# Kernel tuning notes

Hardware: AMD Instinct MI355X
Metric: run time of the kernel (lower is better)

Reference implementation:

```python
import jax, jax.numpy as jnp
import numpy as np

B, S, D, H = 4, 2048, 1024, 16
HD = D // H  # head_dim = 64
SCALE = HD ** -0.5


def setup_inputs() -> dict:
    key = jax.random.key(0)
    k1, k2, k3, k4, k5 = jax.random.split(key, 5)
    std = D ** -0.5
    return {
        "x": jax.random.normal(k1, (B, S, D), dtype=jnp.float32),
        "w_qkv": jax.random.normal(k2, (D, 3 * D), dtype=jnp.float32) * std,
        "b_qkv": jax.random.normal(k3, (3 * D,), dtype=jnp.float32) * 0.01,
        "w_out": jax.random.normal(k4, (D, D), dtype=jnp.float32) * std,
        "b_out": jax.random.normal(k5, (D,), dtype=jnp.float32) * 0.01,
    }


def reference(x, w_qkv, b_qkv, w_out, b_out):
    b, s, d = x.shape
    qkv = x @ w_qkv + b_qkv                                   # [B,S,3D]
    qkv = qkv.reshape(b, s, 3, H, HD).transpose(2, 0, 3, 1, 4)  # [3,B,H,S,HD]
    q, k, v = qkv[0], qkv[1], qkv[2]
    attn = jnp.einsum("bhqd,bhkd->bhqk", q, k) * SCALE        # [B,H,S,S]
    attn = jax.nn.softmax(attn, axis=-1)
    out = jnp.einsum("bhqk,bhkd->bhqd", attn, v)              # [B,H,S,HD]
    out = out.transpose(0, 2, 1, 3).reshape(b, s, d)          # [B,S,D]
    return out @ w_out + b_out
```

## Files before the change

### kernel.cpp

```cpp
#include <hip/hip_runtime.h>
#include <stdint.h>
#include <stddef.h>

#define NB 4
#define NS 2048
#define ND 1024
#define NH 16
#define HDIM 64
#define SCALE 0.125f

typedef __attribute__((ext_vector_type(4))) float f32x4;
typedef __attribute__((ext_vector_type(16))) float f32x16;
typedef __attribute__((ext_vector_type(8))) __bf16 bf16x8;
typedef __attribute__((ext_vector_type(4))) uint32_t u32x4;

__device__ __forceinline__ uint16_t f2bf(float f) {
  uint32_t u = __builtin_bit_cast(uint32_t, f);
  return (uint16_t)((u + 0x7fffu + ((u >> 16) & 1u)) >> 16);
}

__device__ __forceinline__ void gload_lds16(const void* g, void* l) {
  __builtin_amdgcn_global_load_lds((const __attribute__((address_space(1))) void*)g,
                                   (__attribute__((address_space(3))) void*)l, 16, 0, 0);
}

__device__ __forceinline__ uint32_t cvtpk(float lo, float hi) {
  uint32_t r;
  asm("v_cvt_pk_bf16_f32 %0, %1, %2" : "=v"(r) : "v"(lo), "v"(hi));
  return r;
}

__device__ __forceinline__ void permswap(uint32_t& a, uint32_t& b) {
  asm("v_permlane32_swap_b32 %0, %1" : "+v"(a), "+v"(b));
}

__device__ __forceinline__ float fexp2(float x) {
  float r;
  asm("v_exp_f32 %0, %1" : "=v"(r) : "v"(x));
  return r;
}

__global__ void k_cvt_bf16(const float* __restrict__ in, uint16_t* __restrict__ out, int n4) {
  int i = blockIdx.x * blockDim.x + threadIdx.x;
  if (i >= n4) return;
  float4 v = reinterpret_cast<const float4*>(in)[i];
  ushort4 o;
  o.x = f2bf(v.x); o.y = f2bf(v.y); o.z = f2bf(v.z); o.w = f2bf(v.w);
  reinterpret_cast<ushort4*>(out)[i] = o;
}

__global__ void k_transpose_cvt(const float* __restrict__ in, uint16_t* __restrict__ out,
                                int K, int N) {
  __shared__ float tile[64][65];
  const int nb = blockIdx.x * 64, kb = blockIdx.y * 64;
  const int c = threadIdx.x & 63, r0 = threadIdx.x >> 6;
#pragma unroll
  for (int i = 0; i < 16; ++i) {
    int r = r0 * 16 + i;
    tile[r][c] = in[(size_t)(kb + r) * N + nb + c];
  }
  __syncthreads();
#pragma unroll
  for (int i = 0; i < 16; ++i) {
    int rr = r0 * 16 + i;
    out[(size_t)(nb + rr) * K + kb + c] = f2bf(tile[c][rr]);
  }
}

__global__ void k_vt_repack(const uint16_t* __restrict__ qkv, uint16_t* __restrict__ vt) {
  __shared__ uint16_t tile[64][66];
  const int bh = blockIdx.y, sb = blockIdx.x * 64;
  const int b = bh >> 4, h = bh & 15;
  const int c = threadIdx.x & 63, r0 = threadIdx.x >> 6;
#pragma unroll
  for (int i = 0; i < 16; ++i) {
    int s = r0 * 16 + i;
    tile[s][c] = qkv[(size_t)(b * NS + sb + s) * 3072 + 2048 + h * 64 + c];
  }
  __syncthreads();
#pragma unroll
  for (int i = 0; i < 16; ++i) {
    int d = r0 * 16 + i;
    vt[(size_t)bh * 64 * NS + (size_t)d * NS + sb + c] = tile[c][d];
  }
}

template<int OUT_BF16>
__global__ __launch_bounds__(256)
void k_gemm(const uint16_t* __restrict__ A, const uint16_t* __restrict__ Bt,
            const float* __restrict__ bias, void* __restrict__ C,
            int M, int N, int K) {
  __shared__ __align__(16) char Al[8192];
  __shared__ __align__(16) char Bl[8192];
  const int tid = threadIdx.x;
  const int wave = tid >> 6, lane = tid & 63;
  const int mb = blockIdx.y * 128, nb = blockIdx.x * 128;
  const int wm = (wave >> 1) * 64, wn = (wave & 1) * 64;
  const int fr = lane & 15, cc = lane >> 4;
  const int srow = tid >> 2, sch = tid & 3;
  f32x4 acc[4][4] = {};

  for (int kb = 0; kb < K; kb += 32) {
#pragma unroll
    for (int p = 0; p < 2; ++p) {
      int row = p * 64 + srow;
      int cg = sch ^ (row & 3) ^ ((row >> 2) & 3);
      gload_lds16(A + (size_t)(mb + row) * K + kb + cg * 8, Al + p * 4096 + wave * 1024);
      gload_lds16(Bt + (size_t)(nb + row) * K + kb + cg * 8, Bl + p * 4096 + wave * 1024);
    }
    __syncthreads();
    bf16x8 af[4], bfr[4];
#pragma unroll
    for (int i = 0; i < 4; ++i) {
      int ra = wm + i * 16 + fr;
      af[i] = *(const bf16x8*)(Al + ra * 64 + ((cc ^ (ra & 3) ^ ((ra >> 2) & 3)) * 16));
      int rb = wn + i * 16 + fr;
      bfr[i] = *(const bf16x8*)(Bl + rb * 64 + ((cc ^ (rb & 3) ^ ((rb >> 2) & 3)) * 16));
    }
#pragma unroll
    for (int i = 0; i < 4; ++i)
#pragma unroll
      for (int j = 0; j < 4; ++j)
        acc[i][j] = __builtin_amdgcn_mfma_f32_16x16x32_bf16(af[i], bfr[j], acc[i][j], 0, 0, 0);
    __syncthreads();
  }

#pragma unroll
  for (int i = 0; i < 4; ++i)
#pragma unroll
    for (int j = 0; j < 4; ++j)
#pragma unroll
      for (int r = 0; r < 4; ++r) {
        int row = mb + wm + i * 16 + cc * 4 + r;
        int col = nb + wn + j * 16 + fr;
        float v = acc[i][j][r] + bias[col];
        if (OUT_BF16)
          ((uint16_t*)C)[(size_t)row * N + col] = f2bf(v);
        else
          ((float*)C)[(size_t)row * N + col] = v;
      }
}

__global__ __launch_bounds__(256)
void k_attn(const uint16_t* __restrict__ qkv, const uint16_t* __restrict__ vt,
            uint16_t* __restrict__ out) {
  __shared__ __align__(16) char Kl[2][8192];
  __shared__ __align__(16) char Vl[2][8192];

  const int id = blockIdx.y * 16 + blockIdx.x;
  const int wfid = (id & 7) * 128 + (id >> 3);
  const int bh = wfid >> 4, qblk = wfid & 15;
  const int b = bh >> 4, h = bh & 15;
  const int tid = threadIdx.x, wave = tid >> 6, lane = tid & 63;
  const int ln31 = lane & 31, hi = lane >> 5;

  const int q0 = qblk * 128 + wave * 32;
  const uint16_t* qrowp = qkv + (size_t)(b * NS + q0 + ln31) * 3072 + h * 64 + hi * 8;
  bf16x8 qf[4];
#pragma unroll
  for (int kk = 0; kk < 4; ++kk) qf[kk] = *(const bf16x8*)(qrowp + kk * 16);

  const int srow = tid >> 3;
  const int cs = (tid & 7) ^ (srow & 7);
  const uint16_t* ksrc = qkv + (size_t)(b * NS) * 3072 + 1024 + h * 64 + cs * 8;
  const uint16_t* vsrc = vt + (size_t)bh * 64 * NS + cs * 8;

  f32x16 acc0 = {}, acc1 = {};
  float m_run = -1e30f, l_run = 0.f;
  const float C = 0.18033688011112042f;

#pragma unroll
  for (int r = 0; r < 2; ++r) {
    int row = srow + r * 32;
    gload_lds16(ksrc + (size_t)row * 3072, Kl[0] + wave * 1024 + r * 4096);
    gload_lds16(vsrc + (size_t)row * NS, Vl[0] + wave * 1024 + r * 4096);
  }
  __syncthreads();

  const int ksw = ln31 & 7;

  for (int t = 0; t < NS / 64; ++t) {
    const int cur = t & 1;
    if (t < NS / 64 - 1) {
      const int kb2 = (t + 1) * 64;
      char* kd = Kl[cur ^ 1] + wave * 1024;
      char* vd = Vl[cur ^ 1] + wave * 1024;
#pragma unroll
      for (int r = 0; r < 2; ++r) {
        int row = srow + r * 32;
        gload_lds16(ksrc + (size_t)(kb2 + row) * 3072, kd + r * 4096);
        gload_lds16(vsrc + (size_t)row * NS + kb2, vd + r * 4096);
      }
    }

    const char* kb0 = Kl[cur] + ln31 * 128;
    const char* kb1 = kb0 + 32 * 128;
    f32x16 st0 = {}, st1 = {};
#pragma unroll
    for (int kk = 0; kk < 4; ++kk) {
      int c = ((kk * 2 + hi) ^ ksw) * 16;
      bf16x8 k0 = *(const bf16x8*)(kb0 + c);
      bf16x8 k1 = *(const bf16x8*)(kb1 + c);
      st0 = __builtin_amdgcn_mfma_f32_32x32x16_bf16(k0, qf[kk], st0, 0, 0, 0);
      st1 = __builtin_amdgcn_mfma_f32_32x32x16_bf16(k1, qf[kk], st1, 0, 0, 0);
    }

    float mx = st0[0];
#pragma unroll
    for (int r = 1; r < 16; ++r) mx = fmaxf(mx, st0[r]);
#pragma unroll
    for (int r = 0; r < 16; ++r) mx = fmaxf(mx, st1[r]);
    mx = fmaxf(mx, __shfl_xor(mx, 32));
    if (__ballot(mx > m_run + 64.f)) {
      float mn = fmaxf(m_run, mx);
      float al = fexp2((m_run - mn) * C);
      m_run = mn; l_run *= al;
#pragma unroll
      for (int r = 0; r < 16; ++r) { acc0[r] *= al; acc1[r] *= al; }
    }
    const float nmc = -m_run * C;
    float rs = 0.f;
#pragma unroll
    for (int r = 0; r < 16; ++r) { st0[r] = fexp2(fmaf(st0[r], C, nmc)); rs += st0[r]; }
#pragma unroll
    for (int r = 0; r < 16; ++r) { st1[r] = fexp2(fmaf(st1[r], C, nmc)); rs += st1[r]; }
    rs += __shfl_xor(rs, 32);
    l_run += rs;

    const char* vb0 = Vl[cur] + ln31 * 128;
    const char* vb1 = vb0 + 32 * 128;
#pragma unroll
    for (int h2 = 0; h2 < 2; ++h2) {
      f32x16 ph = h2 ? st1 : st0;
#pragma unroll
      for (int s2 = 0; s2 < 2; ++s2) {
        const int kkp = h2 * 2 + s2;
        const int s8 = s2 * 8;
        uint32_t A0 = cvtpk(ph[s8 + 0], ph[s8 + 1]);
        uint32_t A1 = cvtpk(ph[s8 + 2], ph[s8 + 3]);
        uint32_t B0 = cvtpk(ph[s8 + 4], ph[s8 + 5]);
        uint32_t B1 = cvtpk(ph[s8 + 6], ph[s8 + 7]);
        permswap(A0, B0);
        permswap(A1, B1);
        u32x4 pw = {A0, A1, B0, B1};
        bf16x8 pf = __builtin_bit_cast(bf16x8, pw);
        int c = ((kkp * 2 + hi) ^ ksw) * 16;
        bf16x8 v0 = *(const bf16x8*)(vb0 + c);
        bf16x8 v1 = *(const bf16x8*)(vb1 + c);
        acc0 = __builtin_amdgcn_mfma_f32_32x32x16_bf16(v0, pf, acc0, 0, 0, 0);
        acc1 = __builtin_amdgcn_mfma_f32_32x32x16_bf16(v1, pf, acc1, 0, 0, 0);
      }
    }
    __syncthreads();
  }

  const float rl = 1.0f / l_run;
  char* sc = (char*)Kl + wave * 4096 + ln31 * 128;
  const int qsw = ln31 & 15;
#pragma unroll
  for (int dn = 0; dn < 2; ++dn) {
    f32x16 a = dn ? acc1 : acc0;
#pragma unroll
    for (int g = 0; g < 4; ++g) {
      uint2 w;
      w.x = cvtpk(a[4 * g + 0] * rl, a[4 * g + 1] * rl);
      w.y = cvtpk(a[4 * g + 2] * rl, a[4 * g + 3] * rl);
      int c8 = (dn * 8 + 2 * g + hi) ^ qsw;
      *(uint2*)(sc + c8 * 8) = w;
    }
  }
  char* outp = (char*)out + ((size_t)(b * NS + q0 + ln31) * 1024 + h * 64 + hi * 32) * 2;
#pragma unroll
  for (int cc2 = 0; cc2 < 4; ++cc2) {
    uint2 va = *(const uint2*)(sc + (((hi * 8 + 2 * cc2 + 0) ^ qsw) * 8));
    uint2 vb2 = *(const uint2*)(sc + (((hi * 8 + 2 * cc2 + 1) ^ qsw) * 8));
    u32x4 o = {va.x, va.y, vb2.x, vb2.y};
    *(u32x4*)(outp + cc2 * 16) = o;
  }
}

extern "C" void kernel_launch(void* const* d_in, const int* in_sizes, int n_in,
                              void* d_out, int out_size, void* d_ws, size_t ws_size,
                              hipStream_t stream) {
  const float* x     = (const float*)d_in[0];
  const float* w_qkv = (const float*)d_in[1];
  const float* b_qkv = (const float*)d_in[2];
  const float* w_out = (const float*)d_in[3];
  const float* b_out = (const float*)d_in[4];
  float* out = (float*)d_out;
  char* ws = (char*)d_ws;

  uint16_t* Xb    = (uint16_t*)(ws);
  uint16_t* Wqkvt = (uint16_t*)(ws + (16u << 20));
  uint16_t* Woutt = (uint16_t*)(ws + (22u << 20));
  uint16_t* QKV   = (uint16_t*)(ws + (24u << 20));
  uint16_t* Vt    = (uint16_t*)(ws + (72u << 20));
  uint16_t* AO    = Xb;

  k_cvt_bf16<<<(NB * NS * ND / 4 + 255) / 256, 256, 0, stream>>>(x, Xb, NB * NS * ND / 4);
  k_transpose_cvt<<<dim3(48, 16), 256, 0, stream>>>(w_qkv, Wqkvt, ND, 3 * ND);
  k_transpose_cvt<<<dim3(16, 16), 256, 0, stream>>>(w_out, Woutt, ND, ND);
  k_gemm<1><<<dim3(24, 64), 256, 0, stream>>>(Xb, Wqkvt, b_qkv, QKV, NB * NS, 3 * ND, ND);
  k_vt_repack<<<dim3(32, 64), 256, 0, stream>>>(QKV, Vt);
  k_attn<<<dim3(16, 64), 256, 0, stream>>>(QKV, Vt, AO);
  k_gemm<0><<<dim3(8, 64), 256, 0, stream>>>(AO, Woutt, b_out, out, NB * NS, ND, ND);
}
```

Baseline: 229.5 us.

## Add 256x128 double-buffered QKV GEMM with swizzled LDS and raise MFMA priority

Replaces the QKV projection GEMM with a new kernel that uses 256x128 tiles, 512 threads, a 64-wide K step, double-buffered LDS fed by direct global-to-LDS loads with XOR swizzling, and a block-index remap for L2 locality. The aim is more data reuse per tile and loads that overlap MFMA work. It also raises wave priority around the MFMA sections of both this GEMM and the attention kernel. In exchange it uses 96KB of LDS per block, which limits occupancy, and the epilogue writes scalar bf16 values.

Measured after the change: 228.6 us. About the same (-0.4%).

```diff
diff --git a/kernel.cpp b/kernel.cpp
--- a/kernel.cpp
+++ b/kernel.cpp
@@ -83,6 +83,90 @@
     int d = r0 * 16 + i;
     vt[(size_t)bh * 64 * NS + (size_t)d * NS + sb + c] = tile[c][d];
   }
+}
+
+__global__ __launch_bounds__(512, 2)
+void k_gemm256(const uint16_t* __restrict__ A, const uint16_t* __restrict__ Bt,
+               const float* __restrict__ bias, uint16_t* __restrict__ C,
+               int M, int N, int K) {
+  __shared__ __align__(16) char Al[2][32768];
+  __shared__ __align__(16) char Bl[2][16384];
+  const int tid = threadIdx.x, wave = tid >> 6, lane = tid & 63;
+
+  const int flat = blockIdx.y * gridDim.x + blockIdx.x;
+  const int cpx = (gridDim.x * gridDim.y) >> 3;
+  const int swz = (flat & 7) * cpx + (flat >> 3);
+  const int bx = swz % gridDim.x, by = swz / gridDim.x;
+  const int mb = by * 256, nb = bx * 128;
+
+  const int wm = wave >> 1, wn = wave & 1;
+  const int fr = lane & 15, cc = lane >> 4;
+  f32x4 acc[4][4] = {};
+  const int NT = K >> 6;
+
+  const int srow_ = tid >> 3, sslot = tid & 7;
+
+#define STAGE(BUF, KT) do {                                                     \
+    const int kb_ = (KT) * 64;                                                  \
+    _Pragma("unroll")                                                           \
+    for (int i = 0; i < 4; ++i) {                                               \
+      int row = (i * 512 + tid) >> 3;                                           \
+      int ch = sslot ^ (row & 7);                                               \
+      gload_lds16(A + (size_t)(mb + row) * K + kb_ + ch * 8,                    \
+                  Al[BUF] + (size_t)(i * 512 + (wave << 6)) * 16);              \
+    }                                                                           \
+    _Pragma("unroll")                                                           \
+    for (int i = 0; i < 2; ++i) {                                               \
+      int row = (i * 512 + tid) >> 3;                                           \
+      int ch = sslot ^ (row & 7);                                               \
+      gload_lds16(Bt + (size_t)(nb + row) * K + kb_ + ch * 8,                   \
+                  Bl[BUF] + (size_t)(i * 512 + (wave << 6)) * 16);              \
+    }                                                                           \
+  } while (0)
+
+  (void)srow_;
+  STAGE(0, 0);
+  asm volatile("s_waitcnt vmcnt(0)" ::: "memory");
+  __builtin_amdgcn_s_barrier();
+
+  for (int kt = 0; kt < NT; ++kt) {
+    const int cur = kt & 1;
+    if (kt + 1 < NT) STAGE(cur ^ 1, kt + 1);
+
+#pragma unroll
+    for (int ks = 0; ks < 2; ++ks) {
+      bf16x8 af[4], bfg[4];
+#pragma unroll
+      for (int i = 0; i < 4; ++i) {
+        int ra = wm * 64 + i * 16 + fr;
+        af[i] = *(const bf16x8*)(Al[cur] + ra * 128 + (((ks * 4 + cc) ^ (ra & 7)) * 16));
+        int rb = wn * 64 + i * 16 + fr;
+        bfg[i] = *(const bf16x8*)(Bl[cur] + rb * 128 + (((ks * 4 + cc) ^ (rb & 7)) * 16));
+      }
+      __builtin_amdgcn_s_setprio(1);
+#pragma unroll
+      for (int i = 0; i < 4; ++i)
+#pragma unroll
+        for (int j = 0; j < 4; ++j)
+          acc[i][j] = __builtin_amdgcn_mfma_f32_16x16x32_bf16(af[i], bfg[j], acc[i][j], 0, 0, 0);
+      __builtin_amdgcn_s_setprio(0);
+    }
+
+    asm volatile("s_waitcnt vmcnt(0)" ::: "memory");
+    __builtin_amdgcn_s_barrier();
+  }
+#undef STAGE
+
+#pragma unroll
+  for (int i = 0; i < 4; ++i)
+#pragma unroll
+    for (int j = 0; j < 4; ++j)
+#pragma unroll
+      for (int r = 0; r < 4; ++r) {
+        int row = mb + wm * 64 + i * 16 + cc * 4 + r;
+        int col = nb + wn * 64 + j * 16 + fr;
+        C[(size_t)row * N + col] = f2bf(acc[i][j][r] + bias[col]);
+      }
 }
 
 template<int OUT_BF16>
@@ -196,6 +280,7 @@
     const char* kb0 = Kl[cur] + ln31 * 128;
     const char* kb1 = kb0 + 32 * 128;
     f32x16 st0 = {}, st1 = {};
+    __builtin_amdgcn_s_setprio(1);
 #pragma unroll
     for (int kk = 0; kk < 4; ++kk) {
       int c = ((kk * 2 + hi) ^ ksw) * 16;
@@ -204,6 +289,7 @@
       st0 = __builtin_amdgcn_mfma_f32_32x32x16_bf16(k0, qf[kk], st0, 0, 0, 0);
       st1 = __builtin_amdgcn_mfma_f32_32x32x16_bf16(k1, qf[kk], st1, 0, 0, 0);
     }
+    __builtin_amdgcn_s_setprio(0);
 
     float mx = st0[0];
 #pragma unroll
@@ -229,6 +315,7 @@
 
     const char* vb0 = Vl[cur] + ln31 * 128;
     const char* vb1 = vb0 + 32 * 128;
+    __builtin_amdgcn_s_setprio(1);
 #pragma unroll
     for (int h2 = 0; h2 < 2; ++h2) {
       f32x16 ph = h2 ? st1 : st0;
@@ -251,6 +338,8 @@
         acc1 = __builtin_amdgcn_mfma_f32_32x32x16_bf16(v1, pf, acc1, 0, 0, 0);
       }
     }
+    __builtin_amdgcn_s_setprio(0);
+
     __syncthreads();
   }
 
@@ -300,7 +389,7 @@
   k_cvt_bf16<<<(NB * NS * ND / 4 + 255) / 256, 256, 0, stream>>>(x, Xb, NB * NS * ND / 4);
   k_transpose_cvt<<<dim3(48, 16), 256, 0, stream>>>(w_qkv, Wqkvt, ND, 3 * ND);
   k_transpose_cvt<<<dim3(16, 16), 256, 0, stream>>>(w_out, Woutt, ND, ND);
-  k_gemm<1><<<dim3(24, 64), 256, 0, stream>>>(Xb, Wqkvt, b_qkv, QKV, NB * NS, 3 * ND, ND);
+  k_gemm256<<<dim3(24, 32), 512, 0, stream>>>(Xb, Wqkvt, b_qkv, QKV, NB * NS, 3 * ND, ND);
   k_vt_repack<<<dim3(32, 64), 256, 0, stream>>>(QKV, Vt);
   k_attn<<<dim3(16, 64), 256, 0, stream>>>(QKV, Vt, AO);
   k_gemm<0><<<dim3(8, 64), 256, 0, stream>>>(AO, Woutt, b_out, out, NB * NS, ND, ND);
```

## Software-pipeline attention loop: overlap PV of previous tile with softmax of current

Applied to the files above, without the earlier changes.

Restructures the flash-attention main loop so the P·V MFMAs for the previous key tile run interleaved with the max/exp softmax work of the current tile, and the next QK^T is issued right after one barrier per iteration. V gets a third LDS buffer and K/V loads for the tile after next are issued early. s_setprio is raised around the QK MFMA block. The aim is to hide exp/VALU latency behind matrix work, at the cost of more registers (two P fragment sets) and extra LDS.

Result: no change. 229.2 us (-0.1%).

```diff
diff --git a/kernel.cpp b/kernel.cpp
--- a/kernel.cpp
+++ b/kernel.cpp
@@ -145,7 +145,7 @@
 void k_attn(const uint16_t* __restrict__ qkv, const uint16_t* __restrict__ vt,
             uint16_t* __restrict__ out) {
   __shared__ __align__(16) char Kl[2][8192];
-  __shared__ __align__(16) char Vl[2][8192];
+  __shared__ __align__(16) char Vl[3][8192];
 
   const int id = blockIdx.y * 16 + blockIdx.x;
   const int wfid = (id & 7) * 128 + (id >> 3);
@@ -164,102 +164,131 @@
   const int cs = (tid & 7) ^ (srow & 7);
   const uint16_t* ksrc = qkv + (size_t)(b * NS) * 3072 + 1024 + h * 64 + cs * 8;
   const uint16_t* vsrc = vt + (size_t)bh * 64 * NS + cs * 8;
-
-  f32x16 acc0 = {}, acc1 = {};
+  char* const Vbase = (char*)Vl;
+
+  f32x16 st0, st1, acc0 = {}, acc1 = {};
+  bf16x8 pfA[4], pfB[4];
   float m_run = -1e30f, l_run = 0.f;
-  const float C = 0.18033688011112042f;
-
-#pragma unroll
-  for (int r = 0; r < 2; ++r) {
-    int row = srow + r * 32;
-    gload_lds16(ksrc + (size_t)row * 3072, Kl[0] + wave * 1024 + r * 4096);
-    gload_lds16(vsrc + (size_t)row * NS, Vl[0] + wave * 1024 + r * 4096);
-  }
+  const float CL = 0.18033688011112042f;
+  const int ksw = ln31 & 7;
+
+  int vpv = 16384, vstage = 8192, vidle = 0;
+  const uint16_t* kp = ksrc + (size_t)64 * 3072;
+  const uint16_t* vp = vsrc + 64;
+
+#define QK_T(KB) do {                                                        \
+    const char* kb0_ = Kl[KB] + ln31 * 128;                                  \
+    const char* kb1_ = kb0_ + 32 * 128;                                      \
+    _Pragma("unroll")                                                        \
+    for (int r = 0; r < 16; ++r) { st0[r] = 0.f; st1[r] = 0.f; }             \
+    __builtin_amdgcn_s_setprio(1);                                           \
+    _Pragma("unroll")                                                        \
+    for (int kk = 0; kk < 4; ++kk) {                                         \
+      int c_ = ((kk * 2 + hi) ^ ksw) * 16;                                   \
+      bf16x8 k0 = *(const bf16x8*)(kb0_ + c_);                               \
+      bf16x8 k1 = *(const bf16x8*)(kb1_ + c_);                               \
+      st0 = __builtin_amdgcn_mfma_f32_32x32x16_bf16(k0, qf[kk], st0, 0, 0, 0);\
+      st1 = __builtin_amdgcn_mfma_f32_32x32x16_bf16(k1, qf[kk], st1, 0, 0, 0);\
+    }                                                                        \
+    __builtin_amdgcn_s_setprio(0);                                           \
+  } while (0)
+
+#define PV_T(PF, VOFS) do {                                                  \
+    const char* vb0_ = Vbase + (VOFS) + ln31 * 128;                          \
+    const char* vb1_ = vb0_ + 32 * 128;                                      \
+    _Pragma("unroll")                                                        \
+    for (int kkp = 0; kkp < 4; ++kkp) {                                      \
+      int c_ = ((kkp * 2 + hi) ^ ksw) * 16;                                  \
+      bf16x8 v0 = *(const bf16x8*)(vb0_ + c_);                               \
+      bf16x8 v1 = *(const bf16x8*)(vb1_ + c_);                               \
+      acc0 = __builtin_amdgcn_mfma_f32_32x32x16_bf16(v0, PF[kkp], acc0, 0, 0, 0);\
+      acc1 = __builtin_amdgcn_mfma_f32_32x32x16_bf16(v1, PF[kkp], acc1, 0, 0, 0);\
+    }                                                                        \
+  } while (0)
+
+#define PBUILD(DST, SRC, S2) do {                                            \
+    uint32_t A0 = cvtpk(SRC[(S2) * 8 + 0], SRC[(S2) * 8 + 1]);               \
+    uint32_t A1 = cvtpk(SRC[(S2) * 8 + 2], SRC[(S2) * 8 + 3]);               \
+    uint32_t B0 = cvtpk(SRC[(S2) * 8 + 4], SRC[(S2) * 8 + 5]);               \
+    uint32_t B1 = cvtpk(SRC[(S2) * 8 + 6], SRC[(S2) * 8 + 7]);               \
+    permswap(A0, B0); permswap(A1, B1);                                      \
+    u32x4 pw = {A0, A1, B0, B1};                                             \
+    DST = __builtin_bit_cast(bf16x8, pw);                                    \
+  } while (0)
+
+#define BODY(PFPREV, PFCUR, KB, DOPV, DOSTAGE, DOQK) do {                    \
+    if (DOSTAGE) {                                                           \
+      char* kd = Kl[KB] + wave * 1024;                                       \
+      char* vd = Vbase + vstage + wave * 1024;                               \
+      gload_lds16(kp + (size_t)srow * 3072, kd);                             \
+      gload_lds16(kp + (size_t)(srow + 32) * 3072, kd + 4096);               \
+      gload_lds16(vp + (size_t)srow * NS, vd);                               \
+      gload_lds16(vp + (size_t)(srow + 32) * NS, vd + 4096);                 \
+      kp += (size_t)64 * 3072; vp += 64;                                     \
+    }                                                                        \
+        \
+    float mx;                                                                \
+    {                                                                        \
+      float m8[8];                                                           \
+      _Pragma("unroll")                                                      \
+      for (int r = 0; r < 8; ++r)                                            \
+        m8[r] = fmaxf(fmaxf(st0[r], st0[r + 8]), fmaxf(st1[r], st1[r + 8])); \
+      mx = fmaxf(fmaxf(fmaxf(m8[0], m8[4]), fmaxf(m8[1], m8[5])),            \
+                 fmaxf(fmaxf(m8[2], m8[6]), fmaxf(m8[3], m8[7])));           \
+    }                                                                        \
+    if (DOPV) PV_T(PFPREV, vpv);                                             \
+    mx = fmaxf(mx, __shfl_xor(mx, 32));                                      \
+    const bool cond = __ballot(mx > m_run + 64.f) != 0;                      \
+    const float m_new = cond ? fmaxf(m_run, mx) : m_run;                     \
+    const float al = fexp2((m_run - m_new) * CL);  \
+    const float nmc = -m_new * CL;                                           \
+    float rs = 0.f;                                                          \
+    _Pragma("unroll")                                                        \
+    for (int r = 0; r < 16; ++r) { st0[r] = fexp2(fmaf(st0[r], CL, nmc)); rs += st0[r]; } \
+    _Pragma("unroll")                                                        \
+    for (int r = 0; r < 16; ++r) { st1[r] = fexp2(fmaf(st1[r], CL, nmc)); rs += st1[r]; } \
+    rs += __shfl_xor(rs, 32);                                                \
+    PBUILD(PFCUR[0], st0, 0); PBUILD(PFCUR[1], st0, 1);                      \
+    PBUILD(PFCUR[2], st1, 0); PBUILD(PFCUR[3], st1, 1);                      \
+    l_run = l_run * al + rs;                                                 \
+    if (cond) {   \
+      _Pragma("unroll")                                                      \
+      for (int r = 0; r < 16; ++r) { acc0[r] *= al; acc1[r] *= al; }         \
+    }                                                                        \
+    m_run = m_new;                                                           \
+    { int tmp_ = vpv; vpv = vidle; vidle = vstage; vstage = tmp_; }          \
+    if (DOQK) {                                                              \
+      __syncthreads();                                                       \
+      QK_T(KB);                                                              \
+    }                                                                        \
+  } while (0)
+
+  gload_lds16(ksrc + (size_t)srow * 3072, Kl[0] + wave * 1024);
+  gload_lds16(ksrc + (size_t)(srow + 32) * 3072, Kl[0] + wave * 1024 + 4096);
+  gload_lds16(vsrc + (size_t)srow * NS, Vbase + wave * 1024);
+  gload_lds16(vsrc + (size_t)(srow + 32) * NS, Vbase + wave * 1024 + 4096);
   __syncthreads();
-
-  const int ksw = ln31 & 7;
-
-  for (int t = 0; t < NS / 64; ++t) {
-    const int cur = t & 1;
-    if (t < NS / 64 - 1) {
-      const int kb2 = (t + 1) * 64;
-      char* kd = Kl[cur ^ 1] + wave * 1024;
-      char* vd = Vl[cur ^ 1] + wave * 1024;
-#pragma unroll
-      for (int r = 0; r < 2; ++r) {
-        int row = srow + r * 32;
-        gload_lds16(ksrc + (size_t)(kb2 + row) * 3072, kd + r * 4096);
-        gload_lds16(vsrc + (size_t)row * NS + kb2, vd + r * 4096);
-      }
-    }
-
-    const char* kb0 = Kl[cur] + ln31 * 128;
-    const char* kb1 = kb0 + 32 * 128;
-    f32x16 st0 = {}, st1 = {};
-#pragma unroll
-    for (int kk = 0; kk < 4; ++kk) {
-      int c = ((kk * 2 + hi) ^ ksw) * 16;
-      bf16x8 k0 = *(const bf16x8*)(kb0 + c);
-      bf16x8 k1 = *(const bf16x8*)(kb1 + c);
-      st0 = __builtin_amdgcn_mfma_f32_32x32x16_bf16(k0, qf[kk], st0, 0, 0, 0);
-      st1 = __builtin_amdgcn_mfma_f32_32x32x16_bf16(k1, qf[kk], st1, 0, 0, 0);
-    }
-
-    float mx = st0[0];
-#pragma unroll
-    for (int r = 1; r < 16; ++r) mx = fmaxf(mx, st0[r]);
-#pragma unroll
-    for (int r = 0; r < 16; ++r) mx = fmaxf(mx, st1[r]);
-    mx = fmaxf(mx, __shfl_xor(mx, 32));
-    if (__ballot(mx > m_run + 64.f)) {
-      float mn = fmaxf(m_run, mx);
-      float al = fexp2((m_run - mn) * C);
-      m_run = mn; l_run *= al;
-#pragma unroll
-      for (int r = 0; r < 16; ++r) { acc0[r] *= al; acc1[r] *= al; }
-    }
-    const float nmc = -m_run * C;
-    float rs = 0.f;
-#pragma unroll
-    for (int r = 0; r < 16; ++r) { st0[r] = fexp2(fmaf(st0[r], C, nmc)); rs += st0[r]; }
-#pragma unroll
-    for (int r = 0; r < 16; ++r) { st1[r] = fexp2(fmaf(st1[r], C, nmc)); rs += st1[r]; }
-    rs += __shfl_xor(rs, 32);
-    l_run += rs;
-
-    const char* vb0 = Vl[cur] + ln31 * 128;
-    const char* vb1 = vb0 + 32 * 128;
-#pragma unroll
-    for (int h2 = 0; h2 < 2; ++h2) {
-      f32x16 ph = h2 ? st1 : st0;
-#pragma unroll
-      for (int s2 = 0; s2 < 2; ++s2) {
-        const int kkp = h2 * 2 + s2;
-        const int s8 = s2 * 8;
-        uint32_t A0 = cvtpk(ph[s8 + 0], ph[s8 + 1]);
-        uint32_t A1 = cvtpk(ph[s8 + 2], ph[s8 + 3]);
-        uint32_t B0 = cvtpk(ph[s8 + 4], ph[s8 + 5]);
-        uint32_t B1 = cvtpk(ph[s8 + 6], ph[s8 + 7]);
-        permswap(A0, B0);
-        permswap(A1, B1);
-        u32x4 pw = {A0, A1, B0, B1};
-        bf16x8 pf = __builtin_bit_cast(bf16x8, pw);
-        int c = ((kkp * 2 + hi) ^ ksw) * 16;
-        bf16x8 v0 = *(const bf16x8*)(vb0 + c);
-        bf16x8 v1 = *(const bf16x8*)(vb1 + c);
-        acc0 = __builtin_amdgcn_mfma_f32_32x32x16_bf16(v0, pf, acc0, 0, 0, 0);
-        acc1 = __builtin_amdgcn_mfma_f32_32x32x16_bf16(v1, pf, acc1, 0, 0, 0);
-      }
-    }
-    __syncthreads();
-  }
+  QK_T(0);
+
+  BODY(pfB, pfA, 1, 0, 1, 1);
+  for (int t = 1; t < 31; t += 2) {
+    BODY(pfA, pfB, 0, 1, 1, 1);
+    BODY(pfB, pfA, 1, 1, 1, 1);
+  }
+  BODY(pfA, pfB, 0, 1, 0, 0);
+  PV_T(pfB, vpv);
+
+#undef BODY
+#undef PBUILD
+#undef PV_T
+#undef QK_T
 
   const float rl = 1.0f / l_run;
   char* sc = (char*)Kl + wave * 4096 + ln31 * 128;
   const int qsw = ln31 & 15;
 #pragma unroll
   for (int dn = 0; dn < 2; ++dn) {
-    f32x16 a = dn ? acc1 : acc0;
+    const f32x16& a = dn ? acc1 : acc0;
 #pragma unroll
     for (int g = 0; g < 4; ++g) {
       uint2 w;
```
